# Performance work log

Hardware: AMD Instinct MI355X
Metric: run time of the kernel (lower is better)

## Reference

```python
import jax, jax.numpy as jnp
import numpy as np

DEGREE = 7

def setup_inputs() -> dict:
    key = jax.random.key(0)
    k1, k2 = jax.random.split(key)
    input_dims, output_dims = 1024, 1024
    x = jax.random.normal(k1, (8192, input_dims), dtype=jnp.float32)
    std = 1.0 / (input_dims * (DEGREE + 1))
    lucas_coeffs = std * jax.random.normal(k2, (input_dims, output_dims, DEGREE + 1), dtype=jnp.float32)
    return {"x": x, "lucas_coeffs": lucas_coeffs}

def reference(x, lucas_coeffs):
    input_dims = lucas_coeffs.shape[0]
    x = x.reshape(-1, input_dims)
    x = jnp.tanh(x)
    # Lucas polynomial recurrence: L0=2, L1=x, L_i = x*L_{i-1} + L_{i-2}
    basis = [jnp.full_like(x, 2.0)]
    if DEGREE > 0:
        basis.append(x)
    for i in range(2, DEGREE + 1):
        basis.append(x * basis[-1] + basis[-2])
    lucas = jnp.stack(basis, axis=-1)  # [b, i, d]
    y = jnp.einsum('bid,iod->bo', lucas, lucas_coeffs)
    return y
```

## Files before the change

kernel.cpp:

```cpp
#include <hip/hip_runtime.h>
#include <hip/hip_bf16.h>


typedef __attribute__((ext_vector_type(8)))  short  short8;
typedef __attribute__((ext_vector_type(4)))  unsigned short ushort4v;
typedef __attribute__((ext_vector_type(8)))  unsigned short ushort8;
typedef __attribute__((ext_vector_type(4)))  float  float4v;
typedef __attribute__((ext_vector_type(4)))  unsigned int uint4v;

#define M_DIM 8192
#define I_DIM 1024
#define O_DIM 1024
#define K_DIM 8192
#define BM 64
#define BN 128
#define BK 64
#define NSTEP (K_DIM / BK)

__device__ __forceinline__ unsigned short f2bf(float f) {
    unsigned int u = __float_as_uint(f);
    u += 0x7FFFu + ((u >> 16) & 1u);
    return (unsigned short)(u >> 16);
}

__global__ __launch_bounds__(256) void prep_kernel(const float* __restrict__ x,
                                                   const float* __restrict__ c,
                                                   unsigned short* __restrict__ T,
                                                   unsigned short* __restrict__ Bt) {
    int bid = blockIdx.x;
    const int tPart = (M_DIM * I_DIM) / (8 * 256);
    if (bid < tPart) {
        int idx = (bid * 256 + threadIdx.x) * 8;
        float4v v0 = *(const float4v*)(x + idx);
        float4v v1 = *(const float4v*)(x + idx + 4);
        unsigned short t[8];
        t[0] = f2bf(tanhf(v0[0])); t[1] = f2bf(tanhf(v0[1]));
        t[2] = f2bf(tanhf(v0[2])); t[3] = f2bf(tanhf(v0[3]));
        t[4] = f2bf(tanhf(v1[0])); t[5] = f2bf(tanhf(v1[1]));
        t[6] = f2bf(tanhf(v1[2])); t[7] = f2bf(tanhf(v1[3]));
        ushort8 o;
        #pragma unroll
        for (int p = 0; p < 4; ++p) { o[2 * p] = t[p]; o[2 * p + 1] = t[p + 4]; }
        *(ushort8*)(T + idx) = o;
    } else {
        int idx = (bid - tPart) * 256 + threadIdx.x;
        int i = idx >> 10;
        int o = idx & 1023;
        const float* src = c + (size_t)i * 8192 + o * 8;
        float4v lo = *(const float4v*)(src);
        float4v hi = *(const float4v*)(src + 4);
        ushort8 v;
        v[0] = f2bf(lo[0]); v[1] = f2bf(lo[1]); v[2] = f2bf(lo[2]); v[3] = f2bf(lo[3]);
        v[4] = f2bf(hi[0]); v[5] = f2bf(hi[1]); v[6] = f2bf(hi[2]); v[7] = f2bf(hi[3]);
        *(ushort8*)(Bt + (size_t)o * K_DIM + i * 8) = v;
    }
}

__device__ __forceinline__ short8 lucas_frag(unsigned int tb) {
    const float t = __uint_as_float(tb << 16);
    const float L2v = fmaf(t, t, 2.0f);
    const float L3v = fmaf(t, L2v, t);
    const float L4v = fmaf(t, L3v, L2v);
    const float L5v = fmaf(t, L4v, L3v);
    const float L6v = fmaf(t, L5v, L4v);
    const float L7v = fmaf(t, L6v, L5v);
    union { uint4v u; short8 s; } r;
#if __has_builtin(__builtin_amdgcn_cvt_pk_bf16_f32)
    {
        auto p0 = __builtin_amdgcn_cvt_pk_bf16_f32(2.0f, t);
        auto p1 = __builtin_amdgcn_cvt_pk_bf16_f32(L2v, L3v);
        auto p2 = __builtin_amdgcn_cvt_pk_bf16_f32(L4v, L5v);
        auto p3 = __builtin_amdgcn_cvt_pk_bf16_f32(L6v, L7v);
        __builtin_memcpy(&r.u[0], &p0, 4);
        __builtin_memcpy(&r.u[1], &p1, 4);
        __builtin_memcpy(&r.u[2], &p2, 4);
        __builtin_memcpy(&r.u[3], &p3, 4);
    }
#else
    {
        r.u[0] = 0x4000u | (tb << 16);
        r.u[1] = __builtin_amdgcn_perm(__float_as_uint(L3v), __float_as_uint(L2v), 0x07060302);
        r.u[2] = __builtin_amdgcn_perm(__float_as_uint(L5v), __float_as_uint(L4v), 0x07060302);
        r.u[3] = __builtin_amdgcn_perm(__float_as_uint(L7v), __float_as_uint(L6v), 0x07060302);
    }
#endif
    return r.s;
}

__global__ __launch_bounds__(256, 4) void gemm_kernel(const unsigned short* __restrict__ T,
                                                      const unsigned short* __restrict__ Bt,
                                                      float* __restrict__ out) {
    __shared__ unsigned short Bs[2][BN * BK];
    __shared__ unsigned short Ts[2][BM * 8];

    const int tid  = threadIdx.x;
    const int lane = tid & 63;
    const int wave = tid >> 6;
    const int n0 = blockIdx.x * BN;
    const int m0 = blockIdx.y * BM;

    const int wm0  = (wave >> 1) * 32;
    const int wn0  = (wave & 1) * 64;
    const int l16  = lane & 15;
    const int quad = lane >> 4;

    const int srow   = lane >> 3;
    const int il     = lane & 7;
    const int gchunk = il ^ srow;

    float4v acc[2][4];
    const float4v zero = {0.f, 0.f, 0.f, 0.f};
    #pragma unroll
    for (int a = 0; a < 2; ++a)
        #pragma unroll
        for (int b = 0; b < 4; ++b) acc[a][b] = zero;

    #pragma unroll
    for (int r = 0; r < 4; ++r) {
        const int rowb = r * 32 + wave * 8;
        const unsigned short* gB = Bt + (size_t)(n0 + rowb + srow) * K_DIM + gchunk * 8;
        __builtin_amdgcn_global_load_lds(
            (const __attribute__((address_space(1))) unsigned int*)gB,
            (__attribute__((address_space(3))) unsigned int*)&Bs[0][rowb * BK], 16, 0, 0);
    }
    if (wave == 0) {
        const unsigned short* gT = T + (size_t)(m0 + lane) * I_DIM;
        __builtin_amdgcn_global_load_lds(
            (const __attribute__((address_space(1))) unsigned int*)gT,
            (__attribute__((address_space(3))) unsigned int*)&Ts[0][0], 16, 0, 0);
    }
    __syncthreads();

    int cur = 0;
    for (int s = 0; s < NSTEP; ++s) {
        const int nxt = cur ^ 1;

        if (s + 1 < NSTEP) {
            const int kt = (s + 1) * BK;
            #pragma unroll
            for (int r = 0; r < 4; ++r) {
                const int rowb = r * 32 + wave * 8;
                const unsigned short* gB = Bt + (size_t)(n0 + rowb + srow) * K_DIM + kt + gchunk * 8;
                __builtin_amdgcn_global_load_lds(
                    (const __attribute__((address_space(1))) unsigned int*)gB,
                    (__attribute__((address_space(3))) unsigned int*)&Bs[nxt][rowb * BK], 16, 0, 0);
            }
            if (wave == 0) {
                const unsigned short* gT = T + (size_t)(m0 + lane) * I_DIM + kt / 8;
                __builtin_amdgcn_global_load_lds(
                    (const __attribute__((address_space(1))) unsigned int*)gT,
                    (__attribute__((address_space(3))) unsigned int*)&Ts[nxt][0], 16, 0, 0);
            }
        }

        unsigned int tw[2];
        #pragma unroll
        for (int tt = 0; tt < 2; ++tt)
            tw[tt] = *(const unsigned int*)&Ts[cur][(wm0 + tt * 16 + l16) * 8 + quad * 2];

        #pragma unroll
        for (int k2 = 0; k2 < 2; ++k2) {
            short8 af[2];
            af[0] = lucas_frag(k2 ? (tw[0] >> 16) : (tw[0] & 0xffffu));
            af[1] = lucas_frag(k2 ? (tw[1] >> 16) : (tw[1] & 0xffffu));
            short8 bfr[4];
            #pragma unroll
            for (int tn = 0; tn < 4; ++tn) {
                const int brow = wn0 + tn * 16 + l16;
                bfr[tn] = *(const short8*)&Bs[cur][brow * BK + (((k2 * 4 + quad) ^ (l16 & 7)) * 8)];
            }
            #pragma unroll
            for (int tt = 0; tt < 2; ++tt)
                #pragma unroll
                for (int tn = 0; tn < 4; ++tn)
                    acc[tt][tn] = __builtin_amdgcn_mfma_f32_16x16x32_bf16(
                        af[tt], bfr[tn], acc[tt][tn], 0, 0, 0);
        }

        __syncthreads();
        cur = nxt;
    }

    #pragma unroll
    for (int tt = 0; tt < 2; ++tt) {
        #pragma unroll
        for (int tn = 0; tn < 4; ++tn) {
            const int col = n0 + wn0 + tn * 16 + l16;
            #pragma unroll
            for (int r = 0; r < 4; ++r) {
                const int row = m0 + wm0 + tt * 16 + quad * 4 + r;
                out[(size_t)row * O_DIM + col] = acc[tt][tn][r];
            }
        }
    }
}

__global__ __launch_bounds__(256) void naive_kernel(const float* __restrict__ x,
                                                    const float* __restrict__ c,
                                                    float* __restrict__ out) {
    int idx = blockIdx.x * 256 + threadIdx.x;
    int b = idx >> 10;
    int o = idx & 1023;
    const float* xb = x + (size_t)b * I_DIM;
    float acc = 0.f;
    for (int i = 0; i < I_DIM; ++i) {
        float t = tanhf(xb[i]);
        float L[8];
        L[0] = 2.0f; L[1] = t;
        #pragma unroll
        for (int d = 2; d < 8; ++d) L[d] = t * L[d - 1] + L[d - 2];
        const float* cc = c + (size_t)i * 8192 + o * 8;
        #pragma unroll
        for (int d = 0; d < 8; ++d) acc += L[d] * cc[d];
    }
    out[idx] = acc;
}

extern "C" void kernel_launch(void* const* d_in, const int* in_sizes, int n_in,
                              void* d_out, int out_size, void* d_ws, size_t ws_size,
                              hipStream_t stream) {
    const float* x      = (const float*)d_in[0];
    const float* coeffs = (const float*)d_in[1];
    float* out = (float*)d_out;

    const size_t btBytes = (size_t)O_DIM * K_DIM * sizeof(unsigned short);
    const size_t tBytes  = (size_t)M_DIM * I_DIM * sizeof(unsigned short);

    if (ws_size >= btBytes + tBytes) {
        unsigned short* Bt = (unsigned short*)d_ws;
        unsigned short* T  = (unsigned short*)((char*)d_ws + btBytes);

        const int tBlocks = (M_DIM * I_DIM) / (8 * 256);
        const int bBlocks = (I_DIM * O_DIM) / 256;
        prep_kernel<<<tBlocks + bBlocks, 256, 0, stream>>>(x, coeffs, T, Bt);

        dim3 grid(O_DIM / BN, M_DIM / BM);
        gemm_kernel<<<grid, 256, 0, stream>>>(T, Bt, out);
    } else {
        naive_kernel<<<(M_DIM * O_DIM) / 256, 256, 0, stream>>>(x, coeffs, out);
    }
}
```

Measured before the change: 254.3 us.

## Double M tile to 128 and split K in two with atomic accumulation

Grows the block tile from 64x128 to 128x128, so each wave computes a 64x64 sub-tile and reuses every B fragment across four A fragments, cutting B traffic per FLOP. Splits K across two blocks via the grid z dimension to keep the block count unchanged, and combines partial sums with float atomicAdd into an output zeroed by a new kernel. The extra zeroing launch, the atomic traffic, higher register pressure under launch_bounds(256,4), and nondeterministic summation order are the costs.

```diff
diff --git a/kernel.cpp b/kernel.cpp
--- a/kernel.cpp
+++ b/kernel.cpp
@@ -12,15 +12,23 @@
 #define I_DIM 1024
 #define O_DIM 1024
 #define K_DIM 8192
-#define BM 64
+#define BM 128
 #define BN 128
 #define BK 64
-#define NSTEP (K_DIM / BK)
+#define KSPLIT 2
+#define KHALF (K_DIM / KSPLIT)
+#define NSTEP (KHALF / BK)
 
 __device__ __forceinline__ unsigned short f2bf(float f) {
     unsigned int u = __float_as_uint(f);
     u += 0x7FFFu + ((u >> 16) & 1u);
     return (unsigned short)(u >> 16);
+}
+
+__global__ __launch_bounds__(256) void zero_kernel(float* __restrict__ p) {
+    int idx = (blockIdx.x * 256 + threadIdx.x) * 4;
+    const float4v z = {0.f, 0.f, 0.f, 0.f};
+    *(float4v*)(p + idx) = z;
 }
 
 __global__ __launch_bounds__(256) void prep_kernel(const float* __restrict__ x,
@@ -98,8 +106,9 @@
     const int wave = tid >> 6;
     const int n0 = blockIdx.x * BN;
     const int m0 = blockIdx.y * BM;
-
-    const int wm0  = (wave >> 1) * 32;
+    const int k0 = blockIdx.z * KHALF;
+
+    const int wm0  = (wave >> 1) * 64;
     const int wn0  = (wave & 1) * 64;
     const int l16  = lane & 15;
     const int quad = lane >> 4;
@@ -108,26 +117,26 @@
     const int il     = lane & 7;
     const int gchunk = il ^ srow;
 
-    float4v acc[2][4];
+    float4v acc[4][4];
     const float4v zero = {0.f, 0.f, 0.f, 0.f};
     #pragma unroll
-    for (int a = 0; a < 2; ++a)
+    for (int a = 0; a < 4; ++a)
         #pragma unroll
         for (int b = 0; b < 4; ++b) acc[a][b] = zero;
 
     #pragma unroll
     for (int r = 0; r < 4; ++r) {
         const int rowb = r * 32 + wave * 8;
-        const unsigned short* gB = Bt + (size_t)(n0 + rowb + srow) * K_DIM + gchunk * 8;
+        const unsigned short* gB = Bt + (size_t)(n0 + rowb + srow) * K_DIM + k0 + gchunk * 8;
         __builtin_amdgcn_global_load_lds(
             (const __attribute__((address_space(1))) unsigned int*)gB,
             (__attribute__((address_space(3))) unsigned int*)&Bs[0][rowb * BK], 16, 0, 0);
     }
-    if (wave == 0) {
-        const unsigned short* gT = T + (size_t)(m0 + lane) * I_DIM;
+    if (wave < 2) {
+        const unsigned short* gT = T + (size_t)(m0 + wave * 64 + lane) * I_DIM + k0 / 8;
         __builtin_amdgcn_global_load_lds(
             (const __attribute__((address_space(1))) unsigned int*)gT,
-            (__attribute__((address_space(3))) unsigned int*)&Ts[0][0], 16, 0, 0);
+            (__attribute__((address_space(3))) unsigned int*)&Ts[0][wave * 64 * 8], 16, 0, 0);
     }
     __syncthreads();
 
@@ -136,7 +145,7 @@
         const int nxt = cur ^ 1;
 
         if (s + 1 < NSTEP) {
-            const int kt = (s + 1) * BK;
+            const int kt = k0 + (s + 1) * BK;
             #pragma unroll
             for (int r = 0; r < 4; ++r) {
                 const int rowb = r * 32 + wave * 8;
@@ -145,24 +154,21 @@
                     (const __attribute__((address_space(1))) unsigned int*)gB,
                     (__attribute__((address_space(3))) unsigned int*)&Bs[nxt][rowb * BK], 16, 0, 0);
             }
-            if (wave == 0) {
-                const unsigned short* gT = T + (size_t)(m0 + lane) * I_DIM + kt / 8;
+            if (wave < 2) {
+                const unsigned short* gT = T + (size_t)(m0 + wave * 64 + lane) * I_DIM + kt / 8;
                 __builtin_amdgcn_global_load_lds(
                     (const __attribute__((address_space(1))) unsigned int*)gT,
-                    (__attribute__((address_space(3))) unsigned int*)&Ts[nxt][0], 16, 0, 0);
+                    (__attribute__((address_space(3))) unsigned int*)&Ts[nxt][wave * 64 * 8], 16, 0, 0);
             }
         }
 
-        unsigned int tw[2];
-        #pragma unroll
-        for (int tt = 0; tt < 2; ++tt)
+        unsigned int tw[4];
+        #pragma unroll
+        for (int tt = 0; tt < 4; ++tt)
             tw[tt] = *(const unsigned int*)&Ts[cur][(wm0 + tt * 16 + l16) * 8 + quad * 2];
 
         #pragma unroll
         for (int k2 = 0; k2 < 2; ++k2) {
-            short8 af[2];
-            af[0] = lucas_frag(k2 ? (tw[0] >> 16) : (tw[0] & 0xffffu));
-            af[1] = lucas_frag(k2 ? (tw[1] >> 16) : (tw[1] & 0xffffu));
             short8 bfr[4];
             #pragma unroll
             for (int tn = 0; tn < 4; ++tn) {
@@ -170,11 +176,13 @@
                 bfr[tn] = *(const short8*)&Bs[cur][brow * BK + (((k2 * 4 + quad) ^ (l16 & 7)) * 8)];
             }
             #pragma unroll
-            for (int tt = 0; tt < 2; ++tt)
+            for (int tt = 0; tt < 4; ++tt) {
+                const short8 af = lucas_frag(k2 ? (tw[tt] >> 16) : (tw[tt] & 0xffffu));
                 #pragma unroll
                 for (int tn = 0; tn < 4; ++tn)
                     acc[tt][tn] = __builtin_amdgcn_mfma_f32_16x16x32_bf16(
-                        af[tt], bfr[tn], acc[tt][tn], 0, 0, 0);
+                        af, bfr[tn], acc[tt][tn], 0, 0, 0);
+            }
         }
 
         __syncthreads();
@@ -182,14 +190,14 @@
     }
 
     #pragma unroll
-    for (int tt = 0; tt < 2; ++tt) {
+    for (int tt = 0; tt < 4; ++tt) {
         #pragma unroll
         for (int tn = 0; tn < 4; ++tn) {
             const int col = n0 + wn0 + tn * 16 + l16;
             #pragma unroll
             for (int r = 0; r < 4; ++r) {
                 const int row = m0 + wm0 + tt * 16 + quad * 4 + r;
-                out[(size_t)row * O_DIM + col] = acc[tt][tn][r];
+                atomicAdd(&out[(size_t)row * O_DIM + col], acc[tt][tn][r]);
             }
         }
     }
@@ -230,11 +238,13 @@
         unsigned short* Bt = (unsigned short*)d_ws;
         unsigned short* T  = (unsigned short*)((char*)d_ws + btBytes);
 
+        zero_kernel<<<(M_DIM * O_DIM) / (4 * 256), 256, 0, stream>>>(out);
+
         const int tBlocks = (M_DIM * I_DIM) / (8 * 256);
         const int bBlocks = (I_DIM * O_DIM) / 256;
         prep_kernel<<<tBlocks + bBlocks, 256, 0, stream>>>(x, coeffs, T, Bt);
 
-        dim3 grid(O_DIM / BN, M_DIM / BM);
+        dim3 grid(O_DIM / BN, M_DIM / BM, KSPLIT);
         gemm_kernel<<<grid, 256, 0, stream>>>(T, Bt, out);
     } else {
         naive_kernel<<<(M_DIM * O_DIM) / 256, 256, 0, stream>>>(x, coeffs, out);
```

Result: no change. 254.1 us (-0.1%).
